# Performance work log

Measured on AMD Instinct MI355X. Metric: run time of the kernel, lower is better.

Reference implementation:

```python
import jax, jax.numpy as jnp
import numpy as np

H = 128; ED = 16; NF = 200000; EI = 800000; NT = 20000; M = 4; NM = NT * M; EG = 320000; NHEADS = 4


def _ln(x, g, b):
    mu = x.mean(-1, keepdims=True)
    v = ((x - mu) ** 2).mean(-1, keepdims=True)
    return (x - mu) / jnp.sqrt(v + 1e-5) * g + b


def _bn(x, g, b):
    mu = x.mean(0)
    v = ((x - mu) ** 2).mean(0)
    return (x - mu) / jnp.sqrt(v + 1e-5) * g + b


def _gine(x, ei, ea, We, be, W1, b1, W2, b2):
    # GINEConv: msg = relu(x_j + Lin(e_ji)), sum-aggr, eps=0, 2-layer MLP
    msg = jax.nn.relu(x[ei[0]] + ea @ We.T + be)
    agg = jax.ops.segment_sum(msg, ei[1], num_segments=x.shape[0])
    z = x + agg
    return jax.nn.relu(z @ W1.T + b1) @ W2.T + b2


def _view_attn(x, ln1_g, ln1_b, ln2_g, ln2_b, Wqkv, bqkv, Wo, bo, fW1, fb1, fW2, fb2):
    N, m, Hd = x.shape
    dh = Hd // NHEADS
    r = _ln(x, ln1_g, ln1_b)
    qkv = r @ Wqkv.T + bqkv
    q, k, v = jnp.split(qkv, 3, axis=-1)
    q = q.reshape(N, m, NHEADS, dh)
    k = k.reshape(N, m, NHEADS, dh)
    v = v.reshape(N, m, NHEADS, dh)
    s = jnp.einsum('nqhd,nkhd->nhqk', q, k) * (dh ** -0.5)
    a = jax.nn.softmax(s, axis=-1)
    o = jnp.einsum('nhqk,nkhd->nqhd', a, v).reshape(N, m, Hd)
    x = x + o @ Wo.T + bo
    y = _ln(x, ln2_g, ln2_b)
    x = x + jax.nn.gelu(y @ fW1.T + fb1, approximate=False) @ fW2.T + fb2
    return x.mean(axis=1)


def setup_inputs() -> dict:
    key = jax.random.key(0)
    ks = jax.random.split(key, 48)
    rn = lambda i, shape, s=0.02: jax.random.normal(ks[i], shape, jnp.float32) * s
    inp = {}
    inp['h_flat'] = jax.random.normal(ks[0], (NF, H), jnp.float32)
    inp['ea_flat'] = jax.random.normal(ks[1], (EI, ED), jnp.float32)
    inp['edge_attr'] = jax.random.normal(ks[2], (EG, ED), jnp.float32)
    inp['intra_ei'] = jax.random.randint(ks[3], (2, EI), 0, NF)
    inp['edge_index'] = jax.random.randint(ks[4], (2, EG), 0, NT)
    inp['node_ids'] = jax.random.randint(ks[5], (NF,), 0, NT)
    inp['sub_batch'] = jax.random.randint(ks[6], (NF,), 0, NM)
    inp['root_flat_idx'] = jax.random.randint(ks[7], (NM,), 0, NF)
    inp['valid'] = jnp.ones((NF,), jnp.bool_)
    inp['N_total'] = NT
    inp['m'] = M
    inp['Wskip'] = rn(8, (H, H)); inp['bskip'] = jnp.zeros((H,))
    inp['Wvv'] = rn(9, (H, H)); inp['bvv'] = jnp.zeros((H,))
    inp['Wkk'] = rn(10, (H, H)); inp['bkk'] = jnp.zeros((H,))
    inp['lc_We'] = rn(11, (H, ED)); inp['lc_be'] = jnp.zeros((H,))
    inp['lc_W1'] = rn(12, (H, H)); inp['lc_b1'] = jnp.zeros((H,))
    inp['lc_W2'] = rn(13, (H, H)); inp['lc_b2'] = jnp.zeros((H,))
    inp['gc_We'] = rn(14, (H, ED)); inp['gc_be'] = jnp.zeros((H,))
    inp['gc_W1'] = rn(15, (H, H)); inp['gc_b1'] = jnp.zeros((H,))
    inp['gc_W2'] = rn(16, (H, H)); inp['gc_b2'] = jnp.zeros((H,))
    inp['lbn_g'] = jnp.ones((H,)); inp['lbn_b'] = jnp.zeros((H,))
    inp['gbn_g'] = jnp.ones((H,)); inp['gbn_b'] = jnp.zeros((H,))
    inp['ln1_g'] = jnp.ones((H,)); inp['ln1_b'] = jnp.zeros((H,))
    inp['ln2_g'] = jnp.ones((H,)); inp['ln2_b'] = jnp.zeros((H,))
    inp['Wqkv'] = rn(17, (3 * H, H)); inp['bqkv'] = jnp.zeros((3 * H,))
    inp['Wo'] = rn(18, (H, H)); inp['bo'] = jnp.zeros((H,))
    inp['ffn_W1'] = rn(19, (4 * H, H)); inp['ffn_b1'] = jnp.zeros((4 * H,))
    inp['ffn_W2'] = rn(20, (H, 4 * H)); inp['ffn_b2'] = jnp.zeros((H,))
    return inp


def reference(h_flat, ea_flat, edge_attr, intra_ei, edge_index, node_ids, sub_batch,
              root_flat_idx, valid, N_total, m,
              Wskip, bskip, Wvv, bvv, Wkk, bkk,
              lc_We, lc_be, lc_W1, lc_b1, lc_W2, lc_b2,
              gc_We, gc_be, gc_W1, gc_b1, gc_W2, gc_b2,
              lbn_g, lbn_b, gbn_g, gbn_b,
              ln1_g, ln1_b, ln2_g, ln2_b,
              Wqkv, bqkv, Wo, bo, ffn_W1, ffn_b1, ffn_W2, ffn_b2):
    valid_f = valid.astype(jnp.float32)[:, None]                      # [NF,1]
    clamped = jnp.maximum(node_ids, 0)
    valid_mask = (node_ids >= 0).astype(jnp.float32)[:, None]
    h_skip = (h_flat @ Wskip.T + bskip) * valid_f
    h1 = _gine(h_flat, intra_ei, ea_flat, lc_We, lc_be, lc_W1, lc_b1, lc_W2, lc_b2)
    h1 = _bn(h1, lbn_g, lbn_b) * valid_f
    # scatter-mean of valid rows into N_total global nodes
    sums = jax.ops.segment_sum(h_flat * valid_mask, clamped, num_segments=N_total)
    cnt = jax.ops.segment_sum(valid_mask, clamped, num_segments=N_total)
    x_sum = sums / jnp.maximum(cnt, 1.0)
    h_global = _gine(x_sum, edge_index, edge_attr, gc_We, gc_be, gc_W1, gc_b1, gc_W2, gc_b2)
    h2 = _bn(h_global, gbn_g, gbn_b)[clamped] * valid_f
    h_roots3d = h_flat[root_flat_idx].reshape(N_total, m, H)
    x_vv_node = _view_attn(h_roots3d, ln1_g, ln1_b, ln2_g, ln2_b, Wqkv, bqkv, Wo, bo,
                           ffn_W1, ffn_b1, ffn_W2, ffn_b2)
    x_vv = (x_vv_node[clamped] @ Wvv.T + bvv) * valid_f
    x_kk = (h_flat[root_flat_idx[sub_batch]] @ Wkk.T + bkk) * valid_f
    out = jax.nn.relu(h_skip + h1 + h2 + x_vv + x_kk)
    return out * valid_f
```

## Files before the change

### kernel.cpp

```cpp
#include <hip/hip_runtime.h>
#include <math.h>

typedef __bf16 bf16_t;
typedef bf16_t bf16x8 __attribute__((ext_vector_type(8)));
typedef float  f32x4  __attribute__((ext_vector_type(4)));

#define DEV static __device__ __forceinline__

constexpr int H  = 128, ED = 16;
constexpr int NF = 200000, EI = 800000, NT = 20000, MV = 4, NM = NT*MV, EG = 320000;

constexpr int NB_LOCAL = 200192;
constexpr int NB_MEAN  = 20224;
constexpr int NB_GLOB  = 20224;
constexpr int MB_BASE  = NB_LOCAL;
constexpr int GB_BASE  = NB_LOCAL + NB_MEAN;
constexpr int NB       = NB_LOCAL + NB_MEAN + NB_GLOB;
constexpr int NBLK     = NB / 256;
constexpr int TOTW     = EI + NF + EG;

DEV bf16x8 ldb8(const bf16_t* p){ union{uint4 u; bf16x8 v;} t; t.u = *(const uint4*)p; return t.v; }
DEV void   stb8(bf16_t* p, bf16x8 v){ union{uint4 u; bf16x8 f;} t; t.f=v; *(uint4*)p = t.u; }

DEV bf16x8 cvt8(const float* p){
  float4 a = *(const float4*)p, b = *(const float4*)(p+4);
  bf16x8 r;
  r[0]=(bf16_t)a.x; r[1]=(bf16_t)a.y; r[2]=(bf16_t)a.z; r[3]=(bf16_t)a.w;
  r[4]=(bf16_t)b.x; r[5]=(bf16_t)b.y; r[6]=(bf16_t)b.z; r[7]=(bf16_t)b.w;
  return r;
}
DEV bf16x8 cvtadd8(const float* p, const float* q){
  float4 a = *(const float4*)p, b = *(const float4*)(p+4);
  float4 c = *(const float4*)q, d = *(const float4*)(q+4);
  bf16x8 r;
  r[0]=(bf16_t)(a.x+c.x); r[1]=(bf16_t)(a.y+c.y); r[2]=(bf16_t)(a.z+c.z); r[3]=(bf16_t)(a.w+c.w);
  r[4]=(bf16_t)(b.x+d.x); r[5]=(bf16_t)(b.y+d.y); r[6]=(bf16_t)(b.z+d.z); r[7]=(bf16_t)(b.w+d.w);
  return r;
}

struct GArgs {
  const float*  A;      const bf16_t* Abf;   const float* Aadd;  const int* gidx;
  const float*  W;      const float*  bias;
  float*        outf;   bf16_t*       outb;
  const float*  Xadd_f; const bf16_t* Xadd_b; const int* gidx2;
  const bf16_t* B1;     const bf16_t* h2pre; const float* yvv;  const bf16_t* ykk;
  const int*    node_ids; const int*  sub_batch; const float* affine;
  int nrows; int ldout;
};

constexpr int A_F32=0, A_F32_ADD=1, A_BF16=2, A_F32_GATHER=3;
constexpr int E_BIAS_BF16=0, E_RELU_BF16=1, E_GELU_BF16=2, E_BIAS_F32=3,
              E_ADDGATHER_BF16=4, E_ADDROW_BF16=5, E_FINAL=6;

template<int AM>
DEV bf16x8 loadA(const GArgs& g, int row, int koff, int K){
  if constexpr (AM==A_BF16)        return ldb8(g.Abf + (size_t)row*K + koff);
  else if constexpr (AM==A_F32)    return cvt8(g.A   + (size_t)row*K + koff);
  else if constexpr (AM==A_F32_GATHER) return cvt8(g.A + (size_t)g.gidx[row]*K + koff);
  else { size_t o = (size_t)row*K + koff; return cvtadd8(g.A + o, g.Aadd + o); }
}

template<int K, int CTPW, int AM, int EPI>
__global__ __launch_bounds__(256) void k_gemm(GArgs g){
  constexpr int NS = K/32;
  const int lane = threadIdx.x & 63;
  const int wave = threadIdx.x >> 6;
  const int quad = lane >> 4;
  const int r16  = lane & 15;
  const int colBase = (blockIdx.y*4 + wave)*(CTPW*16);

  bf16x8 bfrag[CTPW][NS];
  float  bcol[CTPW];
  #pragma unroll
  for (int c=0;c<CTPW;c++){
    const float* wrow = g.W + (size_t)(colBase + c*16 + r16)*K;
    #pragma unroll
    for (int s=0;s<NS;s++) bfrag[c][s] = cvt8(wrow + s*32 + quad*8);
    bcol[c] = g.bias[colBase + c*16 + r16];
  }
  float aLc[CTPW], bLc[CTPW], aGc[CTPW], bGc[CTPW];
  if constexpr (EPI==E_FINAL){
    #pragma unroll
    for (int c=0;c<CTPW;c++){
      int col = colBase + c*16 + r16;
      aLc[c]=g.affine[col];     bLc[c]=g.affine[128+col];
      aGc[c]=g.affine[256+col]; bGc[c]=g.affine[384+col];
    }
  }

  const int row0 = blockIdx.x*64;
  #pragma unroll 1
  for (int t=0;t<4;t++){
    int rowbase = row0 + t*16;
    if (rowbase >= g.nrows) break;
    int arow = rowbase + r16;
    f32x4 acc[CTPW] = {};
    #pragma unroll
    for (int s=0;s<NS;s++){
      bf16x8 af = loadA<AM>(g, arow, s*32 + quad*8, K);
      #pragma unroll
      for (int c=0;c<CTPW;c++)
        acc[c] = __builtin_amdgcn_mfma_f32_16x16x32_bf16(af, bfrag[c][s], acc[c], 0, 0, 0);
    }
    #pragma unroll
    for (int r=0;r<4;r++){
      int orow = rowbase + quad*4 + r;
      int nid=0, sb=0, g2=0;
      if constexpr (EPI==E_FINAL){ nid = g.node_ids[orow]; sb = g.sub_batch[orow]; }
      if constexpr (EPI==E_ADDGATHER_BF16){ g2 = g.gidx2[orow]; }
      #pragma unroll
      for (int c=0;c<CTPW;c++){
        int col = colBase + c*16 + r16;
        float v = acc[c][r] + bcol[c];
        size_t oidx = (size_t)orow*g.ldout + col;
        if constexpr (EPI==E_BIAS_BF16)      g.outb[oidx] = (bf16_t)v;
        else if constexpr (EPI==E_RELU_BF16) g.outb[oidx] = (bf16_t)fmaxf(v,0.f);
        else if constexpr (EPI==E_GELU_BF16){
          float gv = 0.5f*v*(1.f + erff(v*0.70710678118654752f));
          g.outb[oidx] = (bf16_t)gv;
        }
        else if constexpr (EPI==E_BIAS_F32)  g.outf[oidx] = v;
        else if constexpr (EPI==E_ADDGATHER_BF16){
          v += g.Xadd_f[(size_t)g2*128 + col];
          g.outb[oidx] = (bf16_t)v;
        }
        else if constexpr (EPI==E_ADDROW_BF16){
          v += (float)g.Xadd_b[(size_t)orow*128 + col];
          g.outb[oidx] = (bf16_t)v;
        }
        else if constexpr (EPI==E_FINAL){
          v += (float)g.ykk[(size_t)sb*128 + col];
          v += g.yvv[(size_t)nid*128 + col];
          v += (float)g.B1[(size_t)orow*128 + col]*aLc[c] + bLc[c];
          v += (float)g.h2pre[(size_t)nid*128 + col]*aGc[c] + bGc[c];
          g.outf[oidx] = fmaxf(v, 0.f);
        }
      }
    }
  }
}

__global__ __launch_bounds__(256) void k_hist(const int* eil_dst, const int* nid,
                                              const int* eig_dst, int* cnt){
  int i = blockIdx.x*256 + threadIdx.x;
  if (i < EI)            atomicAdd(&cnt[eil_dst[i]], 1);
  else if (i < EI+NF)    atomicAdd(&cnt[MB_BASE + nid[i-EI]], 1);
  else if (i < TOTW)     atomicAdd(&cnt[GB_BASE + eig_dst[i-EI-NF]], 1);
}

__global__ __launch_bounds__(256) void k_scan1(const int* cnt, int* off, int* bsum){
  __shared__ int s[256];
  int tid = threadIdx.x;
  int i = blockIdx.x*256 + tid;
  int v = cnt[i];
  s[tid] = v; __syncthreads();
  #pragma unroll
  for (int d=1; d<256; d<<=1){
    int t = (tid>=d) ? s[tid-d] : 0;
    __syncthreads();
    s[tid] += t;
    __syncthreads();
  }
  off[i] = s[tid] - v;
  if (tid==255) bsum[blockIdx.x] = s[255];
}

__global__ __launch_bounds__(256) void k_scan2(int* bsum){
  __shared__ int s[NBLK];
  for (int i=threadIdx.x; i<NBLK; i+=256) s[i]=bsum[i];
  __syncthreads();
  if (threadIdx.x==0){
    int run = 0;
    for (int b=0;b<NBLK;b++){
      if (b == NB_LOCAL/256 || b == GB_BASE/256) run = 0;
      int v = s[b]; s[b] = run; run += v;
    }
  }
  __syncthreads();
  for (int i=threadIdx.x; i<NBLK; i+=256) bsum[i]=s[i];
}

__global__ __launch_bounds__(256) void k_scan3(int* off, const int* bsum, int* cur){
  int i = blockIdx.x*256 + threadIdx.x;
  int v = off[i] + bsum[blockIdx.x];
  off[i] = v; cur[i] = v;
}

__global__ __launch_bounds__(256) void k_fill(const int* eil_dst, const int* nid,
                                              const int* eig_dst, int* cur, int* eidx){
  int i = blockIdx.x*256 + threadIdx.x;
  if (i < EI){
    int p = atomicAdd(&cur[eil_dst[i]], 1);
    eidx[p] = i;
  } else if (i < EI+NF){
    int j = i - EI;
    int p = atomicAdd(&cur[MB_BASE + nid[j]], 1);
    eidx[EI + p] = j;
  } else if (i < TOTW){
    int j = i - EI - NF;
    int p = atomicAdd(&cur[GB_BASE + eig_dst[j]], 1);
    eidx[EI + NF + p] = j;
  }
}

__global__ __launch_bounds__(256) void k_gmean(const float* h, const int* off, const int* eidx,
                                               float* xs){
  int wave = threadIdx.x >> 6, lane = threadIdx.x & 63;
  int n = blockIdx.x*4 + wave;
  if (n >= NT) return;
  int o0 = off[MB_BASE + n], o1 = off[MB_BASE + n + 1];
  int c0 = lane*2;
  float ax=0.f, ay=0.f;
  for (int p=o0; p<o1; ++p){
    int r = eidx[EI + p];
    float2 v = *(const float2*)(h + (size_t)r*128 + c0);
    ax += v.x; ay += v.y;
  }
  float inv = 1.f / fmaxf((float)(o1-o0), 1.f);
  float2 o; o.x = ax*inv; o.y = ay*inv;
  *(float2*)(xs + (size_t)n*128 + c0) = o;
}

__global__ __launch_bounds__(256) void k_agg(const float* x, const float* ea, const int* ei_src,
                                             const int* off, const int* eidx,
                                             const float* We, const float* be,
                                             float* agg, int binBase, int eBase, int nrows){
  int wave = threadIdx.x >> 6, lane = threadIdx.x & 63;
  int c0 = lane*2;
  float w0[16], w1[16];
  #pragma unroll
  for (int j=0;j<16;j++){ w0[j] = We[c0*16+j]; w1[j] = We[(c0+1)*16+j]; }
  const float b0 = be[c0], b1 = be[c0+1];
  const int stride = gridDim.x*4;
  for (int r = blockIdx.x*4 + wave; r < nrows; r += stride){
    int o0 = off[binBase + r], o1 = off[binBase + r + 1];
    float ax=0.f, ay=0.f;
    for (int p=o0; p<o1; ++p){
      int e   = eidx[eBase + p];
      int src = ei_src[e];
      float val = ea[(size_t)e*16 + (lane & 15)];
      float d0 = b0, d1 = b1;
      #pragma unroll
      for (int j=0;j<16;j++){
        float a = __shfl(val, j);
        d0 += a*w0[j]; d1 += a*w1[j];
      }
      float2 xs = *(const float2*)(x + (size_t)src*128 + c0);
      ax += fmaxf(xs.x + d0, 0.f);
      ay += fmaxf(xs.y + d1, 0.f);
    }
    float2 o; o.x = ax; o.y = ay;
    *(float2*)(agg + (size_t)r*128 + c0) = o;
  }
}

__global__ __launch_bounds__(256) void k_stats(const bf16_t* X, int nrows, float* stats){
  int c = threadIdx.x & 127, ro = threadIdx.x >> 7;
  int r0 = blockIdx.x*256;
  int rend = (r0+256 < nrows) ? r0+256 : nrows;
  float s1=0.f, s2=0.f;
  for (int i=r0+ro; i<rend; i+=2){
    float v = (float)X[(size_t)i*128 + c];
    s1 += v; s2 += v*v;
  }
  atomicAdd(stats + c,       s1);
  atomicAdd(stats + 128 + c, s2);
}

__global__ void k_affine(const float* sL, const float* sG,
                         const float* lg, const float* lb, const float* gg, const float* gb,
                         float nL, float nG, float* aff){
  int c = threadIdx.x;
  float muL = sL[c]/nL, vL = sL[128+c]/nL - muL*muL;
  float aL = lg[c]*rsqrtf(vL + 1e-5f);
  aff[c] = aL; aff[128+c] = lb[c] - muL*aL;
  float muG = sG[c]/nG, vG = sG[128+c]/nG - muG*muG;
  float aG = gg[c]*rsqrtf(vG + 1e-5f);
  aff[256+c] = aG; aff[384+c] = gb[c] - muG*aG;
}

template<int MODE>
__global__ __launch_bounds__(256) void k_ln(const float* Xf, const bf16_t* Xb, const int* gidx,
                                            const float* gamma, const float* beta, bf16_t* outp, int nrows){
  int wave = threadIdx.x >> 6, lane = threadIdx.x & 63;
  int row = blockIdx.x*4 + wave;
  if (row >= nrows) return;
  int c0 = lane*2;
  float x0, x1;
  if constexpr (MODE==0){
    const float* p = Xf + (size_t)gidx[row]*128;
    x0 = p[c0]; x1 = p[c0+1];
  } else {
    const bf16_t* p = Xb + (size_t)row*128;
    x0 = (float)p[c0]; x1 = (float)p[c0+1];
  }
  float s = x0 + x1, q = x0*x0 + x1*x1;
  #pragma unroll
  for (int m=1; m<64; m<<=1){ s += __shfl_xor(s, m); q += __shfl_xor(q, m); }
  float mu = s*(1.f/128.f);
  float var = q*(1.f/128.f) - mu*mu;
  float rs = rsqrtf(var + 1e-5f);
  outp[(size_t)row*128 + c0]   = (bf16_t)((x0-mu)*rs*gamma[c0]   + beta[c0]);
  outp[(size_t)row*128 + c0+1] = (bf16_t)((x1-mu)*rs*gamma[c0+1] + beta[c0+1]);
}

__global__ __launch_bounds__(256) void k_attn(const bf16_t* qkv, bf16_t* o, int nnodes){
  int wave = threadIdx.x >> 6, lane = threadIdx.x & 63;
  int node = blockIdx.x*4 + wave;
  if (node >= nnodes) return;
  int qv = lane >> 4, hh = (lane >> 2) & 3, sub = lane & 3;
  size_t base = (size_t)node*4*384;
  int coff = hh*32 + sub*8;
  bf16x8 qf = ldb8(qkv + base + (size_t)qv*384 + coff);
  float s[4];
  #pragma unroll
  for (int kv=0;kv<4;kv++){
    bf16x8 kf = ldb8(qkv + base + (size_t)kv*384 + 128 + coff);
    float p = 0.f;
    #pragma unroll
    for (int j=0;j<8;j++) p += (float)qf[j]*(float)kf[j];
    p += __shfl_xor(p, 1);
    p += __shfl_xor(p, 2);
    s[kv] = p * 0.17677669529663687f;
  }
  float mx = fmaxf(fmaxf(s[0],s[1]), fmaxf(s[2],s[3]));
  float e[4]; float sm = 0.f;
  #pragma unroll
  for (int kv=0;kv<4;kv++){ e[kv] = expf(s[kv]-mx); sm += e[kv]; }
  float inv = 1.f/sm;
  float ov[8] = {0,0,0,0,0,0,0,0};
  #pragma unroll
  for (int kv=0;kv<4;kv++){
    float a = e[kv]*inv;
    bf16x8 vf = ldb8(qkv + base + (size_t)kv*384 + 256 + coff);
    #pragma unroll
    for (int j=0;j<8;j++) ov[j] += a*(float)vf[j];
  }
  bf16x8 of;
  #pragma unroll
  for (int j=0;j<8;j++) of[j] = (bf16_t)ov[j];
  stb8(o + (size_t)(node*4+qv)*128 + coff, of);
}

__global__ __launch_bounds__(256) void k_mean(const bf16_t* z2, bf16_t* xvvn){
  int gid = blockIdx.x*256 + threadIdx.x;
  if (gid >= NT*128) return;
  int n = gid >> 7, c = gid & 127;
  size_t b = (size_t)n*4*128 + c;
  float v = (float)z2[b] + (float)z2[b+128] + (float)z2[b+256] + (float)z2[b+384];
  xvvn[(size_t)n*128 + c] = (bf16_t)(v*0.25f);
}

extern "C" void kernel_launch(void* const* d_in, const int* in_sizes, int n_in,
                              void* d_out, int out_size, void* d_ws, size_t ws_size,
                              hipStream_t stream)
{
  const float* h_flat    = (const float*)d_in[0];
  const float* ea_flat   = (const float*)d_in[1];
  const float* edge_attr = (const float*)d_in[2];
  const int*   intra_ei  = (const int*)d_in[3];
  const int*   edge_index= (const int*)d_in[4];
  const int*   node_ids  = (const int*)d_in[5];
  const int*   sub_batch = (const int*)d_in[6];
  const int*   root_idx  = (const int*)d_in[7];
  const float* Wskip = (const float*)d_in[11]; const float* bskip = (const float*)d_in[12];
  const float* Wvv   = (const float*)d_in[13]; const float* bvv   = (const float*)d_in[14];
  const float* Wkk   = (const float*)d_in[15]; const float* bkk   = (const float*)d_in[16];
  const float* lc_We = (const float*)d_in[17]; const float* lc_be = (const float*)d_in[18];
  const float* lc_W1 = (const float*)d_in[19]; const float* lc_b1 = (const float*)d_in[20];
  const float* lc_W2 = (const float*)d_in[21]; const float* lc_b2 = (const float*)d_in[22];
  const float* gc_We = (const float*)d_in[23]; const float* gc_be = (const float*)d_in[24];
  const float* gc_W1 = (const float*)d_in[25]; const float* gc_b1 = (const float*)d_in[26];
  const float* gc_W2 = (const float*)d_in[27]; const float* gc_b2 = (const float*)d_in[28];
  const float* lbn_g = (const float*)d_in[29]; const float* lbn_b = (const float*)d_in[30];
  const float* gbn_g = (const float*)d_in[31]; const float* gbn_b = (const float*)d_in[32];
  const float* ln1_g = (const float*)d_in[33]; const float* ln1_b = (const float*)d_in[34];
  const float* ln2_g = (const float*)d_in[35]; const float* ln2_b = (const float*)d_in[36];
  const float* Wqkv  = (const float*)d_in[37]; const float* bqkv  = (const float*)d_in[38];
  const float* Wo    = (const float*)d_in[39]; const float* bo    = (const float*)d_in[40];
  const float* fW1   = (const float*)d_in[41]; const float* fb1   = (const float*)d_in[42];
  const float* fW2   = (const float*)d_in[43]; const float* fb2   = (const float*)d_in[44];
  float* out = (float*)d_out;

  const int* eil_dst = intra_ei + EI;
  const int* eig_dst = edge_index + EG;

  char* base = (char*)d_ws;
  size_t off_b = 0;
  auto carve = [&](size_t bytes)->char* {
    char* p = base + off_b; off_b += (bytes + 255) & ~(size_t)255; return p;
  };
  float*  agg   = (float*) carve((size_t)NF*H*4);
  bf16_t* qkv   = (bf16_t*)agg;
  bf16_t* tbuf  = (bf16_t*)carve((size_t)NM*512*2);
  bf16_t* mid   = tbuf;
  bf16_t* B1    = (bf16_t*)carve((size_t)NF*H*2);
  bf16_t* rbuf  = (bf16_t*)carve((size_t)NM*H*2);
  bf16_t* z2    = rbuf;
  bf16_t* obuf  = (bf16_t*)carve((size_t)NM*H*2);
  bf16_t* xattn = (bf16_t*)carve((size_t)NM*H*2);
  bf16_t* ykk   = xattn;
  bf16_t* ybuf  = (bf16_t*)carve((size_t)NM*H*2);
  float*  x_sum = (float*) carve((size_t)NT*H*4);
  float*  yvv   = x_sum;
  float*  aggG  = (float*) carve((size_t)NT*H*4);
  bf16_t* tG    = (bf16_t*)carve((size_t)NT*H*2);
  bf16_t* h2pre = (bf16_t*)carve((size_t)NT*H*2);
  bf16_t* xvvn  = (bf16_t*)carve((size_t)NT*H*2);
  float*  statsL= (float*) carve(256*4);
  float*  statsG= (float*) carve(256*4);
  float*  affine= (float*) carve(512*4);
  if (off_b > ws_size) return;

  int* csr      = (int*)tbuf;
  int* cnt_bins = csr;
  int* offs     = cnt_bins + NB;
  int* cur      = offs + NB;
  int* bsum     = cur + NB;
  int* eidx     = bsum + ((NBLK+63)&~63);

  hipMemsetAsync(cnt_bins, 0, (size_t)NB*4, stream);
  hipMemsetAsync(statsL,   0, 2048,         stream);

  auto GX = [](int n){ return (unsigned)((n + 63) / 64); };

  k_hist <<<(TOTW+255)/256, 256, 0, stream>>>(eil_dst, node_ids, eig_dst, cnt_bins);
  k_scan1<<<NBLK, 256, 0, stream>>>(cnt_bins, offs, bsum);
  k_scan2<<<1,    256, 0, stream>>>(bsum);
  k_scan3<<<NBLK, 256, 0, stream>>>(offs, bsum, cur);
  k_fill <<<(TOTW+255)/256, 256, 0, stream>>>(eil_dst, node_ids, eig_dst, cur, eidx);

  k_gmean<<<NT/4, 256, 0, stream>>>(h_flat, offs, eidx, x_sum);
  k_agg  <<<3125, 256, 0, stream>>>(h_flat, ea_flat,   intra_ei,   offs, eidx, lc_We, lc_be,
                                    agg,  0,       0,     NF);
  k_agg  <<<313,  256, 0, stream>>>(x_sum,  edge_attr, edge_index, offs, eidx, gc_We, gc_be,
                                    aggG, GB_BASE, EI+NF, NT);

  { GArgs a{}; a.A=x_sum; a.Aadd=aggG; a.W=gc_W1; a.bias=gc_b1; a.outb=tG; a.nrows=NT; a.ldout=H;
    k_gemm<128,2,A_F32_ADD,E_RELU_BF16><<<dim3(GX(NT),1), 256, 0, stream>>>(a); }
  { GArgs a{}; a.Abf=tG; a.W=gc_W2; a.bias=gc_b2; a.outb=h2pre; a.nrows=NT; a.ldout=H;
    k_gemm<128,2,A_BF16,E_BIAS_BF16><<<dim3(GX(NT),1), 256, 0, stream>>>(a); }
  k_stats<<<(NT+255)/256, 256, 0, stream>>>(h2pre, NT, statsG);
  { GArgs a{}; a.A=h_flat; a.Aadd=agg; a.W=lc_W1; a.bias=lc_b1; a.outb=tbuf; a.nrows=NF; a.ldout=H;
    k_gemm<128,2,A_F32_ADD,E_RELU_BF16><<<dim3(GX(NF),1), 256, 0, stream>>>(a); }
  { GArgs a{}; a.Abf=tbuf; a.W=lc_W2; a.bias=lc_b2; a.outb=B1; a.nrows=NF; a.ldout=H;
    k_gemm<128,2,A_BF16,E_BIAS_BF16><<<dim3(GX(NF),1), 256, 0, stream>>>(a); }
  k_stats<<<(NF+255)/256, 256, 0, stream>>>(B1, NF, statsL);
  k_affine<<<1, 128, 0, stream>>>(statsL, statsG, lbn_g, lbn_b, gbn_g, gbn_b, (float)NF, (float)NT, affine);
  k_ln<0><<<NM/4, 256, 0, stream>>>(h_flat, nullptr, root_idx, ln1_g, ln1_b, rbuf, NM);
  { GArgs a{}; a.Abf=rbuf; a.W=Wqkv; a.bias=bqkv; a.outb=qkv; a.nrows=NM; a.ldout=384;
    k_gemm<128,2,A_BF16,E_BIAS_BF16><<<dim3(GX(NM),3), 256, 0, stream>>>(a); }
  k_attn<<<NT/4, 256, 0, stream>>>(qkv, obuf, NT);
  { GArgs a{}; a.Abf=obuf; a.W=Wo; a.bias=bo; a.Xadd_f=h_flat; a.gidx2=root_idx;
    a.outb=xattn; a.nrows=NM; a.ldout=H;
    k_gemm<128,2,A_BF16,E_ADDGATHER_BF16><<<dim3(GX(NM),1), 256, 0, stream>>>(a); }
  k_ln<1><<<NM/4, 256, 0, stream>>>(nullptr, xattn, nullptr, ln2_g, ln2_b, ybuf, NM);
  { GArgs a{}; a.Abf=ybuf; a.W=fW1; a.bias=fb1; a.outb=mid; a.nrows=NM; a.ldout=512;
    k_gemm<128,2,A_BF16,E_GELU_BF16><<<dim3(GX(NM),4), 256, 0, stream>>>(a); }
  { GArgs a{}; a.Abf=mid; a.W=fW2; a.bias=fb2; a.Xadd_b=xattn; a.outb=z2; a.nrows=NM; a.ldout=H;
    k_gemm<512,1,A_BF16,E_ADDROW_BF16><<<dim3(GX(NM),2), 256, 0, stream>>>(a); }
  k_mean<<<(NT*H)/256, 256, 0, stream>>>(z2, xvvn);
  { GArgs a{}; a.Abf=xvvn; a.W=Wvv; a.bias=bvv; a.outf=yvv; a.nrows=NT; a.ldout=H;
    k_gemm<128,2,A_BF16,E_BIAS_F32><<<dim3(GX(NT),1), 256, 0, stream>>>(a); }
  { GArgs a{}; a.A=h_flat; a.gidx=root_idx; a.W=Wkk; a.bias=bkk; a.outb=ykk; a.nrows=NM; a.ldout=H;
    k_gemm<128,2,A_F32_GATHER,E_BIAS_BF16><<<dim3(GX(NM),1), 256, 0, stream>>>(a); }
  { GArgs a{}; a.A=h_flat; a.W=Wskip; a.bias=bskip; a.outf=out; a.nrows=NF; a.ldout=H;
    a.B1=B1; a.h2pre=h2pre; a.yvv=yvv; a.ykk=ykk;
    a.node_ids=node_ids; a.sub_batch=sub_batch; a.affine=affine;
    k_gemm<128,2,A_F32,E_FINAL><<<dim3(GX(NF),1), 256, 0, stream>>>(a); }
}
```

Baseline: 1.815 ms.

## Precompute edge-linear projections with MFMA in CSR order and aggregate in bf16

Moves the per-edge Linear(edge_attr) out of the aggregation loop into a separate MFMA kernel that writes a bf16 edge-embedding matrix in CSR-sorted order. The aggregation kernel then streams those rows contiguously together with pre-sorted source indices. It unrolls the loop by four with split accumulators and stores agg, x_sum and aggG as bf16. The offsets array is dropped in favour of cursor minus count, and workspace buffers are aliased. In exchange it writes and reads a large EI×128 bf16 intermediate and loses some precision.

```diff
diff --git a/kernel.cpp b/kernel.cpp
--- a/kernel.cpp
+++ b/kernel.cpp
@@ -3,6 +3,7 @@
 
 typedef __bf16 bf16_t;
 typedef bf16_t bf16x8 __attribute__((ext_vector_type(8)));
+typedef bf16_t bf16x2 __attribute__((ext_vector_type(2)));
 typedef float  f32x4  __attribute__((ext_vector_type(4)));
 
 #define DEV static __device__ __forceinline__
@@ -21,6 +22,12 @@
 
 DEV bf16x8 ldb8(const bf16_t* p){ union{uint4 u; bf16x8 v;} t; t.u = *(const uint4*)p; return t.v; }
 DEV void   stb8(bf16_t* p, bf16x8 v){ union{uint4 u; bf16x8 f;} t; t.f=v; *(uint4*)p = t.u; }
+DEV bf16x8 zero8(){
+  bf16x8 z;
+  #pragma unroll
+  for (int j=0;j<8;j++) z[j]=(bf16_t)0.f;
+  return z;
+}
 
 DEV bf16x8 cvt8(const float* p){
   float4 a = *(const float4*)p, b = *(const float4*)(p+4);
@@ -29,17 +36,24 @@
   r[4]=(bf16_t)b.x; r[5]=(bf16_t)b.y; r[6]=(bf16_t)b.z; r[7]=(bf16_t)b.w;
   return r;
 }
-DEV bf16x8 cvtadd8(const float* p, const float* q){
-  float4 a = *(const float4*)p, b = *(const float4*)(p+4);
-  float4 c = *(const float4*)q, d = *(const float4*)(q+4);
-  bf16x8 r;
-  r[0]=(bf16_t)(a.x+c.x); r[1]=(bf16_t)(a.y+c.y); r[2]=(bf16_t)(a.z+c.z); r[3]=(bf16_t)(a.w+c.w);
-  r[4]=(bf16_t)(b.x+d.x); r[5]=(bf16_t)(b.y+d.y); r[6]=(bf16_t)(b.z+d.z); r[7]=(bf16_t)(b.w+d.w);
+DEV bf16x8 cvtaddb(const float* p, const bf16_t* q){
+  float4 a=*(const float4*)p, b=*(const float4*)(p+4);
+  bf16x8 c = ldb8(q), r;
+  r[0]=(bf16_t)(a.x+(float)c[0]); r[1]=(bf16_t)(a.y+(float)c[1]);
+  r[2]=(bf16_t)(a.z+(float)c[2]); r[3]=(bf16_t)(a.w+(float)c[3]);
+  r[4]=(bf16_t)(b.x+(float)c[4]); r[5]=(bf16_t)(b.y+(float)c[5]);
+  r[6]=(bf16_t)(b.z+(float)c[6]); r[7]=(bf16_t)(b.w+(float)c[7]);
   return r;
 }
+DEV bf16x8 addb8(const bf16_t* p, const bf16_t* q){
+  bf16x8 a=ldb8(p), b=ldb8(q), r;
+  #pragma unroll
+  for (int j=0;j<8;j++) r[j]=(bf16_t)((float)a[j]+(float)b[j]);
+  return r;
+}
 
 struct GArgs {
-  const float*  A;      const bf16_t* Abf;   const float* Aadd;  const int* gidx;
+  const float*  A;      const bf16_t* Abf;   const bf16_t* Aadd_b;  const int* gidx;
   const float*  W;      const float*  bias;
   float*        outf;   bf16_t*       outb;
   const float*  Xadd_f; const bf16_t* Xadd_b; const int* gidx2;
@@ -48,16 +62,18 @@
   int nrows; int ldout;
 };
 
-constexpr int A_F32=0, A_F32_ADD=1, A_BF16=2, A_F32_GATHER=3;
+constexpr int A_F32=0, A_F32_ADDB16=1, A_BF16=2, A_F32_GATHER=3, A_B16_ADDB16=4;
 constexpr int E_BIAS_BF16=0, E_RELU_BF16=1, E_GELU_BF16=2, E_BIAS_F32=3,
               E_ADDGATHER_BF16=4, E_ADDROW_BF16=5, E_FINAL=6;
 
 template<int AM>
 DEV bf16x8 loadA(const GArgs& g, int row, int koff, int K){
-  if constexpr (AM==A_BF16)        return ldb8(g.Abf + (size_t)row*K + koff);
-  else if constexpr (AM==A_F32)    return cvt8(g.A   + (size_t)row*K + koff);
+  size_t o = (size_t)row*K + koff;
+  if constexpr (AM==A_BF16)            return ldb8(g.Abf + o);
+  else if constexpr (AM==A_F32)        return cvt8(g.A + o);
   else if constexpr (AM==A_F32_GATHER) return cvt8(g.A + (size_t)g.gidx[row]*K + koff);
-  else { size_t o = (size_t)row*K + koff; return cvtadd8(g.A + o, g.Aadd + o); }
+  else if constexpr (AM==A_F32_ADDB16) return cvtaddb(g.A + o, g.Aadd_b + o);
+  else                                 return addb8(g.Abf + o, g.Aadd_b + o);
 }
 
 template<int K, int CTPW, int AM, int EPI>
@@ -140,6 +156,38 @@
   }
 }
 
+__global__ __launch_bounds__(256) void k_egemm(const float* ea, const int* eidx_seg,
+                                               const float* W, const float* bias,
+                                               bf16_t* E, int nrows){
+  const int lane = threadIdx.x & 63, wave = threadIdx.x >> 6;
+  const int quad = lane >> 4, r16 = lane & 15;
+  const int colBase = wave*32;
+  bf16x8 bfrag[2]; float bcol[2];
+  #pragma unroll
+  for (int c=0;c<2;c++){
+    int col = colBase + c*16 + r16;
+    bfrag[c] = (quad < 2) ? cvt8(W + (size_t)col*16 + quad*8) : zero8();
+    bcol[c] = bias[col];
+  }
+  const int row0 = blockIdx.x*64;
+  #pragma unroll 1
+  for (int t=0;t<4;t++){
+    int rowbase = row0 + t*16;
+    if (rowbase >= nrows) break;
+    int e = eidx_seg[rowbase + r16];
+    bf16x8 af = (quad < 2) ? cvt8(ea + (size_t)e*16 + quad*8) : zero8();
+    f32x4 a0 = {}, a1 = {};
+    a0 = __builtin_amdgcn_mfma_f32_16x16x32_bf16(af, bfrag[0], a0, 0, 0, 0);
+    a1 = __builtin_amdgcn_mfma_f32_16x16x32_bf16(af, bfrag[1], a1, 0, 0, 0);
+    #pragma unroll
+    for (int r=0;r<4;r++){
+      size_t orow = (size_t)(rowbase + quad*4 + r);
+      E[orow*128 + colBase + r16]      = (bf16_t)(a0[r] + bcol[0]);
+      E[orow*128 + colBase + 16 + r16] = (bf16_t)(a1[r] + bcol[1]);
+    }
+  }
+}
+
 __global__ __launch_bounds__(256) void k_hist(const int* eil_dst, const int* nid,
                                               const int* eig_dst, int* cnt){
   int i = blockIdx.x*256 + threadIdx.x;
@@ -148,7 +196,7 @@
   else if (i < TOTW)     atomicAdd(&cnt[GB_BASE + eig_dst[i-EI-NF]], 1);
 }
 
-__global__ __launch_bounds__(256) void k_scan1(const int* cnt, int* off, int* bsum){
+__global__ __launch_bounds__(256) void k_scan1(const int* cnt, int* cur, int* bsum){
   __shared__ int s[256];
   int tid = threadIdx.x;
   int i = blockIdx.x*256 + tid;
@@ -161,7 +209,7 @@
     s[tid] += t;
     __syncthreads();
   }
-  off[i] = s[tid] - v;
+  cur[i] = s[tid] - v;
   if (tid==255) bsum[blockIdx.x] = s[255];
 }
 
@@ -180,18 +228,19 @@
   for (int i=threadIdx.x; i<NBLK; i+=256) bsum[i]=s[i];
 }
 
-__global__ __launch_bounds__(256) void k_scan3(int* off, const int* bsum, int* cur){
+__global__ __launch_bounds__(256) void k_scan3(int* cur, const int* bsum){
   int i = blockIdx.x*256 + threadIdx.x;
-  int v = off[i] + bsum[blockIdx.x];
-  off[i] = v; cur[i] = v;
-}
-
-__global__ __launch_bounds__(256) void k_fill(const int* eil_dst, const int* nid,
-                                              const int* eig_dst, int* cur, int* eidx){
+  cur[i] += bsum[blockIdx.x];
+}
+
+__global__ __launch_bounds__(256) void k_fill(const int* eil_src, const int* eil_dst,
+                                              const int* nid,
+                                              const int* eig_src, const int* eig_dst,
+                                              int* cur, int* eidx, int* srcsL, int* srcsG){
   int i = blockIdx.x*256 + threadIdx.x;
   if (i < EI){
     int p = atomicAdd(&cur[eil_dst[i]], 1);
-    eidx[p] = i;
+    eidx[p] = i;  srcsL[p] = eil_src[i];
   } else if (i < EI+NF){
     int j = i - EI;
     int p = atomicAdd(&cur[MB_BASE + nid[j]], 1);
@@ -199,58 +248,83 @@
   } else if (i < TOTW){
     int j = i - EI - NF;
     int p = atomicAdd(&cur[GB_BASE + eig_dst[j]], 1);
-    eidx[EI + NF + p] = j;
-  }
-}
-
-__global__ __launch_bounds__(256) void k_gmean(const float* h, const int* off, const int* eidx,
-                                               float* xs){
+    eidx[EI + NF + p] = j;  srcsG[p] = eig_src[j];
+  }
+}
+
+__global__ __launch_bounds__(256) void k_gmean(const float* h, const int* cur, const int* cnt,
+                                               const int* eidx, bf16_t* xs){
   int wave = threadIdx.x >> 6, lane = threadIdx.x & 63;
   int n = blockIdx.x*4 + wave;
   if (n >= NT) return;
-  int o0 = off[MB_BASE + n], o1 = off[MB_BASE + n + 1];
+  int o1 = cur[MB_BASE+n], d = cnt[MB_BASE+n], o0 = o1 - d;
   int c0 = lane*2;
-  float ax=0.f, ay=0.f;
-  for (int p=o0; p<o1; ++p){
-    int r = eidx[EI + p];
-    float2 v = *(const float2*)(h + (size_t)r*128 + c0);
-    ax += v.x; ay += v.y;
-  }
-  float inv = 1.f / fmaxf((float)(o1-o0), 1.f);
-  float2 o; o.x = ax*inv; o.y = ay*inv;
-  *(float2*)(xs + (size_t)n*128 + c0) = o;
-}
-
-__global__ __launch_bounds__(256) void k_agg(const float* x, const float* ea, const int* ei_src,
-                                             const int* off, const int* eidx,
-                                             const float* We, const float* be,
-                                             float* agg, int binBase, int eBase, int nrows){
+  float a0=0,a1=0,b0=0,b1=0;
+  int p = o0;
+  for (; p+4<=o1; p+=4){
+    int r0=eidx[EI+p], r1=eidx[EI+p+1], r2=eidx[EI+p+2], r3=eidx[EI+p+3];
+    float2 v0=*(const float2*)(h+(size_t)r0*128+c0);
+    float2 v1=*(const float2*)(h+(size_t)r1*128+c0);
+    float2 v2=*(const float2*)(h+(size_t)r2*128+c0);
+    float2 v3=*(const float2*)(h+(size_t)r3*128+c0);
+    a0+=v0.x; a1+=v0.y; b0+=v1.x; b1+=v1.y;
+    a0+=v2.x; a1+=v2.y; b0+=v3.x; b1+=v3.y;
+  }
+  for (; p<o1; ++p){
+    int r=eidx[EI+p];
+    float2 v=*(const float2*)(h+(size_t)r*128+c0);
+    a0+=v.x; a1+=v.y;
+  }
+  float inv = 1.f/fmaxf((float)d,1.f);
+  bf16x2 o; o[0]=(bf16_t)((a0+b0)*inv); o[1]=(bf16_t)((a1+b1)*inv);
+  *(bf16x2*)(xs+(size_t)n*128+c0) = o;
+}
+
+template<int XF32>
+__global__ __launch_bounds__(256) void k_agg2(const void* xv, const bf16_t* E, const int* srcs,
+                                              const int* cnt, const int* cur, int binBase,
+                                              bf16_t* agg, int nrows){
+  const float* xf=(const float*)xv; const bf16_t* xb=(const bf16_t*)xv;
   int wave = threadIdx.x >> 6, lane = threadIdx.x & 63;
   int c0 = lane*2;
-  float w0[16], w1[16];
-  #pragma unroll
-  for (int j=0;j<16;j++){ w0[j] = We[c0*16+j]; w1[j] = We[(c0+1)*16+j]; }
-  const float b0 = be[c0], b1 = be[c0+1];
-  const int stride = gridDim.x*4;
-  for (int r = blockIdx.x*4 + wave; r < nrows; r += stride){
-    int o0 = off[binBase + r], o1 = off[binBase + r + 1];
-    float ax=0.f, ay=0.f;
-    for (int p=o0; p<o1; ++p){
-      int e   = eidx[eBase + p];
-      int src = ei_src[e];
-      float val = ea[(size_t)e*16 + (lane & 15)];
-      float d0 = b0, d1 = b1;
-      #pragma unroll
-      for (int j=0;j<16;j++){
-        float a = __shfl(val, j);
-        d0 += a*w0[j]; d1 += a*w1[j];
+  int stride = gridDim.x*4;
+  for (int r = blockIdx.x*4+wave; r < nrows; r += stride){
+    int o1 = cur[binBase+r], d = cnt[binBase+r];
+    int p = o1 - d;
+    float a0=0,a1=0,b0=0,b1=0;
+    for (; p+4<=o1; p+=4){
+      int s0=srcs[p], s1=srcs[p+1], s2=srcs[p+2], s3=srcs[p+3];
+      bf16x2 e0=*(const bf16x2*)(E+(size_t)(p  )*128+c0);
+      bf16x2 e1=*(const bf16x2*)(E+(size_t)(p+1)*128+c0);
+      bf16x2 e2=*(const bf16x2*)(E+(size_t)(p+2)*128+c0);
+      bf16x2 e3=*(const bf16x2*)(E+(size_t)(p+3)*128+c0);
+      float x00,x01,x10,x11,x20,x21,x30,x31;
+      if constexpr (XF32){
+        float2 v0=*(const float2*)(xf+(size_t)s0*128+c0); x00=v0.x; x01=v0.y;
+        float2 v1=*(const float2*)(xf+(size_t)s1*128+c0); x10=v1.x; x11=v1.y;
+        float2 v2=*(const float2*)(xf+(size_t)s2*128+c0); x20=v2.x; x21=v2.y;
+        float2 v3=*(const float2*)(xf+(size_t)s3*128+c0); x30=v3.x; x31=v3.y;
+      } else {
+        bf16x2 v0=*(const bf16x2*)(xb+(size_t)s0*128+c0); x00=(float)v0[0]; x01=(float)v0[1];
+        bf16x2 v1=*(const bf16x2*)(xb+(size_t)s1*128+c0); x10=(float)v1[0]; x11=(float)v1[1];
+        bf16x2 v2=*(const bf16x2*)(xb+(size_t)s2*128+c0); x20=(float)v2[0]; x21=(float)v2[1];
+        bf16x2 v3=*(const bf16x2*)(xb+(size_t)s3*128+c0); x30=(float)v3[0]; x31=(float)v3[1];
       }
-      float2 xs = *(const float2*)(x + (size_t)src*128 + c0);
-      ax += fmaxf(xs.x + d0, 0.f);
-      ay += fmaxf(xs.y + d1, 0.f);
-    }
-    float2 o; o.x = ax; o.y = ay;
-    *(float2*)(agg + (size_t)r*128 + c0) = o;
+      a0+=fmaxf(x00+(float)e0[0],0.f); a1+=fmaxf(x01+(float)e0[1],0.f);
+      b0+=fmaxf(x10+(float)e1[0],0.f); b1+=fmaxf(x11+(float)e1[1],0.f);
+      a0+=fmaxf(x20+(float)e2[0],0.f); a1+=fmaxf(x21+(float)e2[1],0.f);
+      b0+=fmaxf(x30+(float)e3[0],0.f); b1+=fmaxf(x31+(float)e3[1],0.f);
+    }
+    for (; p<o1; ++p){
+      int s=srcs[p];
+      bf16x2 e=*(const bf16x2*)(E+(size_t)p*128+c0);
+      float xx0,xx1;
+      if constexpr (XF32){ float2 v=*(const float2*)(xf+(size_t)s*128+c0); xx0=v.x; xx1=v.y; }
+      else { bf16x2 v=*(const bf16x2*)(xb+(size_t)s*128+c0); xx0=(float)v[0]; xx1=(float)v[1]; }
+      a0+=fmaxf(xx0+(float)e[0],0.f); a1+=fmaxf(xx1+(float)e[1],0.f);
+    }
+    bf16x2 o; o[0]=(bf16_t)(a0+b0); o[1]=(bf16_t)(a1+b1);
+    *(bf16x2*)(agg+(size_t)r*128+c0) = o;
   }
 }
 
@@ -382,71 +456,80 @@
   const float* fW2   = (const float*)d_in[43]; const float* fb2   = (const float*)d_in[44];
   float* out = (float*)d_out;
 
-  const int* eil_dst = intra_ei + EI;
-  const int* eig_dst = edge_index + EG;
+  const int* eil_src = intra_ei;          const int* eil_dst = intra_ei + EI;
+  const int* eig_src = edge_index;        const int* eig_dst = edge_index + EG;
 
   char* base = (char*)d_ws;
   size_t off_b = 0;
   auto carve = [&](size_t bytes)->char* {
     char* p = base + off_b; off_b += (bytes + 255) & ~(size_t)255; return p;
   };
-  float*  agg   = (float*) carve((size_t)NF*H*4);
-  bf16_t* qkv   = (bf16_t*)agg;
-  bf16_t* tbuf  = (bf16_t*)carve((size_t)NM*512*2);
-  bf16_t* mid   = tbuf;
-  bf16_t* B1    = (bf16_t*)carve((size_t)NF*H*2);
-  bf16_t* rbuf  = (bf16_t*)carve((size_t)NM*H*2);
+  char* R1 = carve((size_t)EI*128*2);
+  bf16_t* E_L   = (bf16_t*)R1;
+  bf16_t* E_G   = (bf16_t*)R1;
+  bf16_t* B1    = (bf16_t*)R1;
+  bf16_t* xattn = (bf16_t*)(R1 +  51200000);
+  bf16_t* ykk   = xattn;
+  bf16_t* rbuf  = (bf16_t*)(R1 +  71680000);
+  bf16_t* obuf  = rbuf;
   bf16_t* z2    = rbuf;
-  bf16_t* obuf  = (bf16_t*)carve((size_t)NM*H*2);
-  bf16_t* xattn = (bf16_t*)carve((size_t)NM*H*2);
-  bf16_t* ykk   = xattn;
-  bf16_t* ybuf  = (bf16_t*)carve((size_t)NM*H*2);
-  float*  x_sum = (float*) carve((size_t)NT*H*4);
-  float*  yvv   = x_sum;
-  float*  aggG  = (float*) carve((size_t)NT*H*4);
-  bf16_t* tG    = (bf16_t*)carve((size_t)NT*H*2);
-  bf16_t* h2pre = (bf16_t*)carve((size_t)NT*H*2);
-  bf16_t* xvvn  = (bf16_t*)carve((size_t)NT*H*2);
+  bf16_t* ybuf  = (bf16_t*)(R1 +  92160000);
+  bf16_t* tbuf  = (bf16_t*)(R1 +  92160000);
+  bf16_t* mid   = (bf16_t*)(R1 + 112640000);
+  float*  yvv   = (float*) (R1 + 194560000);
+  char* R2 = carve((size_t)NM*384*2);
+  bf16_t* agg = (bf16_t*)R2;
+  bf16_t* qkv = (bf16_t*)R2;
+  char* R3 = carve(((size_t)(NB*2 + 1024 + (EI+NF+EG) + EI + EG))*4);
+  int* cnt_bins = (int*)R3;
+  int* cur      = cnt_bins + NB;
+  int* bsum     = cur + NB;
+  int* eidx     = bsum + 1024;
+  int* srcsL    = eidx + (EI+NF+EG);
+  int* srcsG    = srcsL + EI;
+  bf16_t* x_sum = (bf16_t*)carve((size_t)NT*128*2);
+  bf16_t* aggG  = (bf16_t*)carve((size_t)NT*128*2);
+  bf16_t* tG    = (bf16_t*)carve((size_t)NT*128*2);
+  bf16_t* h2pre = (bf16_t*)carve((size_t)NT*128*2);
+  bf16_t* xvvn  = (bf16_t*)carve((size_t)NT*128*2);
   float*  statsL= (float*) carve(256*4);
   float*  statsG= (float*) carve(256*4);
   float*  affine= (float*) carve(512*4);
   if (off_b > ws_size) return;
 
-  int* csr      = (int*)tbuf;
-  int* cnt_bins = csr;
-  int* offs     = cnt_bins + NB;
-  int* cur      = offs + NB;
-  int* bsum     = cur + NB;
-  int* eidx     = bsum + ((NBLK+63)&~63);
-
-  hipMemsetAsync(cnt_bins, 0, (size_t)NB*4, stream);
-  hipMemsetAsync(statsL,   0, 2048,         stream);
+  (void)hipMemsetAsync(cnt_bins, 0, (size_t)NB*4, stream);
+  (void)hipMemsetAsync(statsL,   0, 2048,         stream);
 
   auto GX = [](int n){ return (unsigned)((n + 63) / 64); };
 
   k_hist <<<(TOTW+255)/256, 256, 0, stream>>>(eil_dst, node_ids, eig_dst, cnt_bins);
-  k_scan1<<<NBLK, 256, 0, stream>>>(cnt_bins, offs, bsum);
+  k_scan1<<<NBLK, 256, 0, stream>>>(cnt_bins, cur, bsum);
   k_scan2<<<1,    256, 0, stream>>>(bsum);
-  k_scan3<<<NBLK, 256, 0, stream>>>(offs, bsum, cur);
-  k_fill <<<(TOTW+255)/256, 256, 0, stream>>>(eil_dst, node_ids, eig_dst, cur, eidx);
-
-  k_gmean<<<NT/4, 256, 0, stream>>>(h_flat, offs, eidx, x_sum);
-  k_agg  <<<3125, 256, 0, stream>>>(h_flat, ea_flat,   intra_ei,   offs, eidx, lc_We, lc_be,
-                                    agg,  0,       0,     NF);
-  k_agg  <<<313,  256, 0, stream>>>(x_sum,  edge_attr, edge_index, offs, eidx, gc_We, gc_be,
-                                    aggG, GB_BASE, EI+NF, NT);
-
-  { GArgs a{}; a.A=x_sum; a.Aadd=aggG; a.W=gc_W1; a.bias=gc_b1; a.outb=tG; a.nrows=NT; a.ldout=H;
-    k_gemm<128,2,A_F32_ADD,E_RELU_BF16><<<dim3(GX(NT),1), 256, 0, stream>>>(a); }
+  k_scan3<<<NBLK, 256, 0, stream>>>(cur, bsum);
+  k_fill <<<(TOTW+255)/256, 256, 0, stream>>>(eil_src, eil_dst, node_ids, eig_src, eig_dst,
+                                              cur, eidx, srcsL, srcsG);
+
+  k_gmean<<<NT/4, 256, 0, stream>>>(h_flat, cur, cnt_bins, eidx, x_sum);
+
+  k_egemm<<<EI/64, 256, 0, stream>>>(ea_flat, eidx, lc_We, lc_be, E_L, EI);
+  k_agg2<1><<<NF/16, 256, 0, stream>>>(h_flat, E_L, srcsL, cnt_bins, cur, 0, agg, NF);
+
+  k_egemm<<<EG/64, 256, 0, stream>>>(edge_attr, eidx + EI + NF, gc_We, gc_be, E_G, EG);
+  k_agg2<0><<<NT/4, 256, 0, stream>>>(x_sum, E_G, srcsG, cnt_bins, cur, GB_BASE, aggG, NT);
+
+  { GArgs a{}; a.Abf=x_sum; a.Aadd_b=aggG; a.W=gc_W1; a.bias=gc_b1; a.outb=tG; a.nrows=NT; a.ldout=H;
+    k_gemm<128,2,A_B16_ADDB16,E_RELU_BF16><<<dim3(GX(NT),1), 256, 0, stream>>>(a); }
   { GArgs a{}; a.Abf=tG; a.W=gc_W2; a.bias=gc_b2; a.outb=h2pre; a.nrows=NT; a.ldout=H;
     k_gemm<128,2,A_BF16,E_BIAS_BF16><<<dim3(GX(NT),1), 256, 0, stream>>>(a); }
   k_stats<<<(NT+255)/256, 256, 0, stream>>>(h2pre, NT, statsG);
-  { GArgs a{}; a.A=h_flat; a.Aadd=agg; a.W=lc_W1; a.bias=lc_b1; a.outb=tbuf; a.nrows=NF; a.ldout=H;
-    k_gemm<128,2,A_F32_ADD,E_RELU_BF16><<<dim3(GX(NF),1), 256, 0, stream>>>(a); }
+
+  { GArgs a{}; a.A=h_flat; a.Aadd_b=agg; a.W=lc_W1; a.bias=lc_b1; a.outb=tbuf; a.nrows=NF; a.ldout=H;
+    k_gemm<128,2,A_F32_ADDB16,E_RELU_BF16><<<dim3(GX(NF),1), 256, 0, stream>>>(a); }
   { GArgs a{}; a.Abf=tbuf; a.W=lc_W2; a.bias=lc_b2; a.outb=B1; a.nrows=NF; a.ldout=H;
     k_gemm<128,2,A_BF16,E_BIAS_BF16><<<dim3(GX(NF),1), 256, 0, stream>>>(a); }
   k_stats<<<(NF+255)/256, 256, 0, stream>>>(B1, NF, statsL);
   k_affine<<<1, 128, 0, stream>>>(statsL, statsG, lbn_g, lbn_b, gbn_g, gbn_b, (float)NF, (float)NT, affine);
+
   k_ln<0><<<NM/4, 256, 0, stream>>>(h_flat, nullptr, root_idx, ln1_g, ln1_b, rbuf, NM);
   { GArgs a{}; a.Abf=rbuf; a.W=Wqkv; a.bias=bqkv; a.outb=qkv; a.nrows=NM; a.ldout=384;
     k_gemm<128,2,A_BF16,E_BIAS_BF16><<<dim3(GX(NM),3), 256, 0, stream>>>(a); }
```

After: 1.549 ms. -14.7%, faster.
